# Kernel tuning notes

Hardware: AMD Instinct MI355X
Metric: run time of the kernel (lower is better)

The kernel has to match this reference:

```python
import jax, jax.numpy as jnp
import numpy as np


def _silu(x):
    return x * jax.nn.sigmoid(x)


def setup_inputs() -> dict:
    key = jax.random.key(0)
    ks = jax.random.split(key, 8)
    B, S, H, E, I, IS = 2, 1024, 2048, 64, 512, 1024
    s = 0.02  # weight init scale to keep activations in a sane range
    return {
        "hidden_states": jax.random.normal(ks[0], (B, S, H), jnp.float32),
        "gate_weight": jax.random.normal(ks[1], (E, H), jnp.float32) * s,   # router [E,H]
        "w_gate": jax.random.normal(ks[2], (E, H, I), jnp.float32) * s,
        "w_up": jax.random.normal(ks[3], (E, H, I), jnp.float32) * s,
        "w_down": jax.random.normal(ks[4], (E, I, H), jnp.float32) * s,
        "sw_gate": jax.random.normal(ks[5], (H, IS), jnp.float32) * s,
        "sw_up": jax.random.normal(ks[6], (H, IS), jnp.float32) * s,
        "sw_down": jax.random.normal(ks[7], (IS, H), jnp.float32) * s,
        "top_k": 6,
    }


def reference(hidden_states, gate_weight, w_gate, w_up, w_down,
              sw_gate, sw_up, sw_down, top_k):
    orig_shape = hidden_states.shape
    H = orig_shape[-1]
    x = hidden_states.reshape(-1, H)          # [T,H]
    T = x.shape[0]
    E = gate_weight.shape[0]

    # fp32 router (need_fp32_gate)
    logits = x.astype(jnp.float32) @ gate_weight.astype(jnp.float32).T   # [T,E]
    # sigmoid_routing_function: sigmoid -> normalize -> topk -> renormalize
    p = jax.nn.sigmoid(logits)
    p = p / jnp.sum(p, axis=-1, keepdims=True)
    topk_w, topk_idx = jax.lax.top_k(p, top_k)                           # [T,k]
    topk_w = topk_w / jnp.sum(topk_w, axis=-1, keepdims=True)            # renormalize

    # dense combine weights [T,E]: zero for unselected experts
    cw = jnp.zeros((T, E), x.dtype).at[jnp.arange(T)[:, None], topk_idx].set(
        topk_w.astype(x.dtype))

    # grouped SwiGLU expert FFN, combine weighted outputs; scan over experts
    # keeps peak memory at one [T,I] intermediate per step.
    def step(acc, ew):
        wg, wu, wd, c = ew                                               # c: [T]
        y = (_silu(x @ wg) * (x @ wu)) @ wd                              # [T,H]
        return acc + c[:, None] * y, None

    routed, _ = jax.lax.scan(step, jnp.zeros_like(x),
                             (w_gate, w_up, w_down, cw.T))

    # shared experts FFN over all tokens (returned separately, not reduced)
    shared_out = (_silu(x @ sw_gate) * (x @ sw_up)) @ sw_down            # [T,H]

    return shared_out, routed.reshape(orig_shape)
```

## Files before the change

kernel.cpp:

```cpp
#include <hip/hip_runtime.h>
#include <hip/hip_bf16.h>
#include <stdint.h>


#define H_DIM 2048
#define E_NUM 64
#define I_DIM 512
#define IS_DIM 1024
#define CAP 512
#define TOPK_MAX 8
#define BK 128
#define LDP 136

typedef float f32x4 __attribute__((ext_vector_type(4)));
typedef __bf16 bf16x8 __attribute__((ext_vector_type(8)));

__device__ __forceinline__ uint16_t f2bf(float f) {
  union { float f; uint32_t u; } v;
  v.f = f;
  uint32_t r = (v.u + 0x7FFFu + ((v.u >> 16) & 1u)) >> 16;
  return (uint16_t)r;
}
__device__ __forceinline__ uint32_t pack2(float a, float b) {
  return (uint32_t)f2bf(a) | ((uint32_t)f2bf(b) << 16);
}
__device__ __forceinline__ float bf2f(uint16_t b) {
  union { uint32_t u; float f; } v;
  v.u = (uint32_t)b << 16;
  return v.f;
}

__global__ __launch_bounds__(256) void router_kernel(
    const float* __restrict__ x, const float* __restrict__ gw,
    const int* __restrict__ topk_ptr, int* __restrict__ cnt,
    int* __restrict__ bucket, float* __restrict__ bw,
    uint16_t* __restrict__ xb) {
  const int t = blockIdx.x;
  const int tid = threadIdx.x;
  __shared__ float xs[H_DIM];
  __shared__ float logits[E_NUM];
#pragma unroll
  for (int i = 0; i < 2; ++i) {
    int idx = tid + i * 256;
    *(float4*)(&xs[idx * 4]) = *(const float4*)(x + (size_t)t * H_DIM + idx * 4);
  }
  __syncthreads();
  {
    const float* p = &xs[tid * 8];
    uint4 o;
    o.x = pack2(p[0], p[1]);
    o.y = pack2(p[2], p[3]);
    o.z = pack2(p[4], p[5]);
    o.w = pack2(p[6], p[7]);
    ((uint4*)(xb + (size_t)t * H_DIM))[tid] = o;
  }
  const int lane = tid & 63, wid = tid >> 6;
  float xr[32];
#pragma unroll
  for (int it = 0; it < 32; ++it) xr[it] = xs[lane + 64 * it];
  for (int eo = 0; eo < 16; ++eo) {
    int e = wid + eo * 4;
    const float* g = gw + (size_t)e * H_DIM;
    float acc = 0.f;
#pragma unroll
    for (int it = 0; it < 32; ++it) acc += xr[it] * g[lane + 64 * it];
#pragma unroll
    for (int off = 32; off; off >>= 1) acc += __shfl_xor(acc, off);
    if (lane == 0) logits[e] = acc;
  }
  __syncthreads();
  if (wid == 0) {
    int k = topk_ptr[0];
    if (k > TOPK_MAX) k = TOPK_MAX;
    float v = 1.f / (1.f + expf(-logits[lane]));
    float s = 0.f, myw = 0.f;
    int mye = 0;
    for (int j = 0; j < k; ++j) {
      float m = v;
      int mi = lane;
#pragma unroll
      for (int off = 32; off; off >>= 1) {
        float ov = __shfl_xor(m, off);
        int oi = __shfl_xor(mi, off);
        if (ov > m || (ov == m && oi < mi)) { m = ov; mi = oi; }
      }
      if (lane == j) { myw = m; mye = mi; }
      if (lane == mi) v = -1e30f;
      s += m;
    }
    if (lane < k) {
      float w = myw / s;
      int pos = atomicAdd(&cnt[mye], 1);
      if (pos < CAP) {
        bucket[mye * CAP + pos] = t * 8 + lane;
        bw[mye * CAP + pos] = w;
      }
    }
  }
}

template <int BM, int BN, bool GATHER>
__global__ __launch_bounds__(256) void ffn_in(
    const uint16_t* __restrict__ xb, const float* __restrict__ Wg,
    const float* __restrict__ Wu, uint16_t* __restrict__ act,
    const int* __restrict__ cnt, const int* __restrict__ bucket,
    const int K, const int ldb) {
  constexpr int MF = BM / 64;
  constexpr int NF = BN / 16;
  constexpr int CG = BN / 4;
  constexpr int PG = 256 / CG;
  constexpr int PAIRS = (BK / 2) / PG;

  int e = 0, nt, mt0, mtE, n_e;
  const float *Bg, *Bu;
  uint16_t* actE;
  if constexpr (GATHER) {
    e = blockIdx.x;
    nt = blockIdx.y;
    n_e = min(cnt[e], CAP);
    mt0 = 0;
    mtE = (n_e + BM - 1) / BM;
    const size_t wo = (size_t)e * K * ldb;
    Bg = Wg + wo;
    Bu = Wu + wo;
    actE = act + (size_t)e * CAP * ldb;
  } else {
    nt = blockIdx.x;
    mt0 = blockIdx.y;
    mtE = mt0 + 1;
    n_e = gridDim.y * BM;
    Bg = Wg;
    Bu = Wu;
    actE = act;
  }
  if (mt0 * BM >= n_e) return;

  __shared__ uint16_t Bgs[BN][LDP];
  __shared__ uint16_t Bus[BN][LDP];

  const int tid = threadIdx.x;
  const int bcol = (tid % CG) * 4, brow = tid / CG;
  const float* bgp = Bg + (size_t)(2 * brow) * ldb + nt * BN + bcol;
  const float* bup = Bu + (size_t)(2 * brow) * ldb + nt * BN + bcol;

  const int lane = tid & 63, wid = tid >> 6;
  const int fr = lane & 15, kg = lane >> 4;

  for (int mt = mt0; mt < mtE; ++mt) {
    const uint16_t* ab[MF];
#pragma unroll
    for (int mf = 0; mf < MF; ++mf) {
      const int slot = mt * BM + wid * (BM / 4) + mf * 16 + fr;
      if constexpr (GATHER) {
        const int idx = slot < n_e ? slot : 0;
        const int bv = bucket[e * CAP + idx];
        ab[mf] = xb + (size_t)(bv >> 3) * K + kg * 8;
      } else {
        ab[mf] = xb + (size_t)slot * K + kg * 8;
      }
    }

    f32x4 accg[MF][NF] = {};
    f32x4 accu[MF][NF] = {};

    float4 g0[PAIRS], g1[PAIRS], u0[PAIRS], u1[PAIRS];
#pragma unroll
    for (int pp = 0; pp < PAIRS; ++pp) {
      const float* g = bgp + (size_t)(2 * pp * PG) * ldb;
      g0[pp] = *(const float4*)g;
      g1[pp] = *(const float4*)(g + ldb);
      const float* u = bup + (size_t)(2 * pp * PG) * ldb;
      u0[pp] = *(const float4*)u;
      u1[pp] = *(const float4*)(u + ldb);
    }

    for (int k0 = 0; k0 < K; k0 += BK) {
      __syncthreads();
#pragma unroll
      for (int pp = 0; pp < PAIRS; ++pp) {
        const int rr2 = 2 * (brow + pp * PG);
        *(uint32_t*)(&Bgs[bcol + 0][rr2]) = pack2(g0[pp].x, g1[pp].x);
        *(uint32_t*)(&Bgs[bcol + 1][rr2]) = pack2(g0[pp].y, g1[pp].y);
        *(uint32_t*)(&Bgs[bcol + 2][rr2]) = pack2(g0[pp].z, g1[pp].z);
        *(uint32_t*)(&Bgs[bcol + 3][rr2]) = pack2(g0[pp].w, g1[pp].w);
        *(uint32_t*)(&Bus[bcol + 0][rr2]) = pack2(u0[pp].x, u1[pp].x);
        *(uint32_t*)(&Bus[bcol + 1][rr2]) = pack2(u0[pp].y, u1[pp].y);
        *(uint32_t*)(&Bus[bcol + 2][rr2]) = pack2(u0[pp].z, u1[pp].z);
        *(uint32_t*)(&Bus[bcol + 3][rr2]) = pack2(u0[pp].w, u1[pp].w);
      }
      __syncthreads();
      if (k0 + BK < K) {
#pragma unroll
        for (int pp = 0; pp < PAIRS; ++pp) {
          const float* g = bgp + (size_t)(k0 + BK + 2 * pp * PG) * ldb;
          g0[pp] = *(const float4*)g;
          g1[pp] = *(const float4*)(g + ldb);
          const float* u = bup + (size_t)(k0 + BK + 2 * pp * PG) * ldb;
          u0[pp] = *(const float4*)u;
          u1[pp] = *(const float4*)(u + ldb);
        }
      }
#pragma unroll
      for (int kk = 0; kk < BK / 32; ++kk) {
        bf16x8 af[MF];
#pragma unroll
        for (int mf = 0; mf < MF; ++mf)
          af[mf] = __builtin_bit_cast(
              bf16x8, *(const uint4*)(ab[mf] + k0 + kk * 32));
#pragma unroll
        for (int nf = 0; nf < NF; ++nf) {
          const bf16x8 bg = __builtin_bit_cast(
              bf16x8, *(const uint4*)(&Bgs[nf * 16 + fr][kg * 8 + kk * 32]));
          const bf16x8 bu = __builtin_bit_cast(
              bf16x8, *(const uint4*)(&Bus[nf * 16 + fr][kg * 8 + kk * 32]));
#pragma unroll
          for (int mf = 0; mf < MF; ++mf) {
            accg[mf][nf] = __builtin_amdgcn_mfma_f32_16x16x32_bf16(
                af[mf], bg, accg[mf][nf], 0, 0, 0);
            accu[mf][nf] = __builtin_amdgcn_mfma_f32_16x16x32_bf16(
                af[mf], bu, accu[mf][nf], 0, 0, 0);
          }
        }
      }
    }

#pragma unroll
    for (int mf = 0; mf < MF; ++mf)
#pragma unroll
      for (int rr = 0; rr < 4; ++rr) {
        const int slot = mt * BM + wid * (BM / 4) + mf * 16 + kg * 4 + rr;
        if (slot < n_e) {
          const size_t ro = (size_t)slot * ldb + nt * BN + fr;
#pragma unroll
          for (int nf = 0; nf < NF; ++nf) {
            const float g = accg[mf][nf][rr], u = accu[mf][nf][rr];
            actE[ro + nf * 16] = f2bf(g / (1.f + expf(-g)) * u);
          }
        }
      }
  }
}

template <int BM, int BN, bool GATHER>
__global__ __launch_bounds__(256) void ffn_down(
    const uint16_t* __restrict__ act, const float* __restrict__ Wd,
    void* __restrict__ outp, const int* __restrict__ cnt,
    const int* __restrict__ bucket, const float* __restrict__ bw, const int K) {
  constexpr int MF = BM / 64;
  constexpr int NF = BN / 16;
  constexpr int CG = BN / 4;
  constexpr int PG = 256 / CG;
  constexpr int PAIRS = (BK / 2) / PG;

  int e = 0, nt, mt0, mtE, n_e;
  const float* Bd;
  const uint16_t* actE;
  if constexpr (GATHER) {
    e = blockIdx.x;
    nt = blockIdx.y;
    n_e = min(cnt[e], CAP);
    mt0 = 0;
    mtE = (n_e + BM - 1) / BM;
    actE = act + (size_t)e * CAP * K;
    Bd = Wd + (size_t)e * K * H_DIM;
  } else {
    nt = blockIdx.x;
    mt0 = blockIdx.y;
    mtE = mt0 + 1;
    n_e = gridDim.y * BM;
    actE = act;
    Bd = Wd;
  }
  if (mt0 * BM >= n_e) return;

  __shared__ uint16_t Bs[BN][LDP];

  const int tid = threadIdx.x;
  const int bcol = (tid % CG) * 4, brow = tid / CG;
  const float* bdp = Bd + (size_t)(2 * brow) * H_DIM + nt * BN + bcol;

  const int lane = tid & 63, wid = tid >> 6;
  const int fr = lane & 15, kg = lane >> 4;

  for (int mt = mt0; mt < mtE; ++mt) {
    const uint16_t* ab[MF];
#pragma unroll
    for (int mf = 0; mf < MF; ++mf) {
      const int slot = mt * BM + wid * (BM / 4) + mf * 16 + fr;
      const int idx = slot < n_e ? slot : 0;
      ab[mf] = actE + (size_t)idx * K + kg * 8;
    }

    f32x4 acc[MF][NF] = {};

    float4 d0[PAIRS], d1[PAIRS];
#pragma unroll
    for (int pp = 0; pp < PAIRS; ++pp) {
      const float* d = bdp + (size_t)(2 * pp * PG) * H_DIM;
      d0[pp] = *(const float4*)d;
      d1[pp] = *(const float4*)(d + H_DIM);
    }

    for (int k0 = 0; k0 < K; k0 += BK) {
      __syncthreads();
#pragma unroll
      for (int pp = 0; pp < PAIRS; ++pp) {
        const int rr2 = 2 * (brow + pp * PG);
        *(uint32_t*)(&Bs[bcol + 0][rr2]) = pack2(d0[pp].x, d1[pp].x);
        *(uint32_t*)(&Bs[bcol + 1][rr2]) = pack2(d0[pp].y, d1[pp].y);
        *(uint32_t*)(&Bs[bcol + 2][rr2]) = pack2(d0[pp].z, d1[pp].z);
        *(uint32_t*)(&Bs[bcol + 3][rr2]) = pack2(d0[pp].w, d1[pp].w);
      }
      __syncthreads();
      if (k0 + BK < K) {
#pragma unroll
        for (int pp = 0; pp < PAIRS; ++pp) {
          const float* d = bdp + (size_t)(k0 + BK + 2 * pp * PG) * H_DIM;
          d0[pp] = *(const float4*)d;
          d1[pp] = *(const float4*)(d + H_DIM);
        }
      }
#pragma unroll
      for (int kk = 0; kk < BK / 32; ++kk) {
        bf16x8 af[MF];
#pragma unroll
        for (int mf = 0; mf < MF; ++mf)
          af[mf] = __builtin_bit_cast(
              bf16x8, *(const uint4*)(ab[mf] + k0 + kk * 32));
#pragma unroll
        for (int nf = 0; nf < NF; ++nf) {
          const bf16x8 bf_ = __builtin_bit_cast(
              bf16x8, *(const uint4*)(&Bs[nf * 16 + fr][kg * 8 + kk * 32]));
#pragma unroll
          for (int mf = 0; mf < MF; ++mf)
            acc[mf][nf] = __builtin_amdgcn_mfma_f32_16x16x32_bf16(
                af[mf], bf_, acc[mf][nf], 0, 0, 0);
        }
      }
    }

    const int col0 = nt * BN + fr;
#pragma unroll
    for (int mf = 0; mf < MF; ++mf)
#pragma unroll
      for (int rr = 0; rr < 4; ++rr) {
        const int slot = mt * BM + wid * (BM / 4) + mf * 16 + kg * 4 + rr;
        if constexpr (GATHER) {
          if (slot < n_e) {
            const int bv = bucket[e * CAP + slot];
            const float w = bw[e * CAP + slot];
            uint16_t* yb = (uint16_t*)outp + (size_t)bv * H_DIM + col0;
#pragma unroll
            for (int nf = 0; nf < NF; ++nf)
              yb[nf * 16] = f2bf(w * acc[mf][nf][rr]);
          }
        } else {
          float* op = (float*)outp + (size_t)slot * H_DIM + col0;
#pragma unroll
          for (int nf = 0; nf < NF; ++nf) op[nf * 16] = acc[mf][nf][rr];
        }
      }
  }
}

__global__ __launch_bounds__(256) void gather_kernel(
    const uint16_t* __restrict__ ybuf, const int* __restrict__ topk_ptr,
    float* __restrict__ routed) {
  const int t = blockIdx.x;
  const int tid = threadIdx.x;
  int k = topk_ptr[0];
  if (k > TOPK_MAX) k = TOPK_MAX;
  float acc[8] = {};
  const uint16_t* base = ybuf + (size_t)t * 8 * H_DIM + tid * 8;
  for (int j = 0; j < k; ++j) {
    uint4 v = *(const uint4*)(base + (size_t)j * H_DIM);
    const uint16_t* h = (const uint16_t*)&v;
#pragma unroll
    for (int i = 0; i < 8; ++i) acc[i] += bf2f(h[i]);
  }
  float4 o0 = make_float4(acc[0], acc[1], acc[2], acc[3]);
  float4 o1 = make_float4(acc[4], acc[5], acc[6], acc[7]);
  float* op = routed + (size_t)t * H_DIM + tid * 8;
  *(float4*)op = o0;
  *(float4*)(op + 4) = o1;
}

extern "C" void kernel_launch(void* const* d_in, const int* in_sizes, int n_in,
                              void* d_out, int out_size, void* d_ws, size_t ws_size,
                              hipStream_t stream) {
  const float* x = (const float*)d_in[0];
  const float* gw = (const float*)d_in[1];
  const float* w_gate = (const float*)d_in[2];
  const float* w_up = (const float*)d_in[3];
  const float* w_down = (const float*)d_in[4];
  const float* sw_gate = (const float*)d_in[5];
  const float* sw_up = (const float*)d_in[6];
  const float* sw_down = (const float*)d_in[7];
  const int* topk = (const int*)d_in[8];
  const int T = in_sizes[0] / H_DIM;

  float* shared_out = (float*)d_out;
  float* routed = shared_out + (size_t)T * H_DIM;

  char* ws = (char*)d_ws;
  size_t off = 0;
  auto take = [&](size_t b) {
    char* p = ws + off;
    off += (b + 255) & ~(size_t)255;
    return p;
  };
  uint16_t* xb = (uint16_t*)take((size_t)T * H_DIM * 2);
  int* cnt = (int*)take(E_NUM * 4);
  int* bucket = (int*)take((size_t)E_NUM * CAP * 4);
  float* bw = (float*)take((size_t)E_NUM * CAP * 4);
  uint16_t* act = (uint16_t*)take((size_t)E_NUM * CAP * I_DIM * 2);
  uint16_t* s_act = (uint16_t*)take((size_t)T * IS_DIM * 2);
  uint16_t* ybuf = (uint16_t*)take((size_t)T * 8 * H_DIM * 2);

  hipMemsetAsync(cnt, 0, E_NUM * 4, stream);

  router_kernel<<<T, 256, 0, stream>>>(x, gw, topk, cnt, bucket, bw, xb);

  ffn_in<256, 32, true><<<dim3(E_NUM, I_DIM / 32), 256, 0, stream>>>(
      xb, w_gate, w_up, act, cnt, bucket, H_DIM, I_DIM);
  ffn_down<256, 64, true><<<dim3(E_NUM, H_DIM / 64), 256, 0, stream>>>(
      act, w_down, (void*)ybuf, cnt, bucket, bw, I_DIM);
  gather_kernel<<<T, 256, 0, stream>>>(ybuf, topk, routed);
  ffn_in<64, 64, false><<<dim3(IS_DIM / 64, T / 64), 256, 0, stream>>>(
      xb, sw_gate, sw_up, s_act, nullptr, nullptr, H_DIM, IS_DIM);
  ffn_down<64, 128, false><<<dim3(H_DIM / 128, T / 64), 256, 0, stream>>>(
      s_act, sw_down, (void*)shared_out, nullptr, nullptr, nullptr, IS_DIM);
}
```

Baseline: 506.8 us.

## Load weight fragments directly from global memory, dropping LDS staging in FFN kernels

Removes the shared-memory staging of fp32 weights (with its pack-to-bf16 writes and two barriers per K tile). Each lane now reads its B fragment straight from global memory as 8 strided scalar fp32 loads and converts them in registers. Warps are rearranged into a 2x2 grid over M and N, and the shared-expert tile shapes and launch order change. This removes sync and LDS overhead but gives up cross-warp reuse of weight loads. The strided scalar global loads are poorly coalesced and may raise memory traffic.

```diff
diff --git a/kernel.cpp b/kernel.cpp
--- a/kernel.cpp
+++ b/kernel.cpp
@@ -9,8 +9,6 @@
 #define IS_DIM 1024
 #define CAP 512
 #define TOPK_MAX 8
-#define BK 128
-#define LDP 136
 
 typedef float f32x4 __attribute__((ext_vector_type(4)));
 typedef __bf16 bf16x8 __attribute__((ext_vector_type(8)));
@@ -105,11 +103,8 @@
     const float* __restrict__ Wu, uint16_t* __restrict__ act,
     const int* __restrict__ cnt, const int* __restrict__ bucket,
     const int K, const int ldb) {
-  constexpr int MF = BM / 64;
-  constexpr int NF = BN / 16;
-  constexpr int CG = BN / 4;
-  constexpr int PG = 256 / CG;
-  constexpr int PAIRS = (BK / 2) / PG;
+  constexpr int MF = BM / 32;
+  constexpr int NF = BN / 32;
 
   int e = 0, nt, mt0, mtE, n_e;
   const float *Bg, *Bu;
@@ -135,22 +130,19 @@
   }
   if (mt0 * BM >= n_e) return;
 
-  __shared__ uint16_t Bgs[BN][LDP];
-  __shared__ uint16_t Bus[BN][LDP];
-
   const int tid = threadIdx.x;
-  const int bcol = (tid % CG) * 4, brow = tid / CG;
-  const float* bgp = Bg + (size_t)(2 * brow) * ldb + nt * BN + bcol;
-  const float* bup = Bu + (size_t)(2 * brow) * ldb + nt * BN + bcol;
-
   const int lane = tid & 63, wid = tid >> 6;
+  const int wm = wid >> 1, wn = wid & 1;
   const int fr = lane & 15, kg = lane >> 4;
+
+  const float* bgp = Bg + (size_t)(kg * 8) * ldb + nt * BN + wn * (BN / 2) + fr;
+  const float* bup = Bu + (size_t)(kg * 8) * ldb + nt * BN + wn * (BN / 2) + fr;
 
   for (int mt = mt0; mt < mtE; ++mt) {
     const uint16_t* ab[MF];
 #pragma unroll
     for (int mf = 0; mf < MF; ++mf) {
-      const int slot = mt * BM + wid * (BM / 4) + mf * 16 + fr;
+      const int slot = mt * BM + wm * (BM / 2) + mf * 16 + fr;
       if constexpr (GATHER) {
         const int idx = slot < n_e ? slot : 0;
         const int bv = bucket[e * CAP + idx];
@@ -163,74 +155,45 @@
     f32x4 accg[MF][NF] = {};
     f32x4 accu[MF][NF] = {};
 
-    float4 g0[PAIRS], g1[PAIRS], u0[PAIRS], u1[PAIRS];
-#pragma unroll
-    for (int pp = 0; pp < PAIRS; ++pp) {
-      const float* g = bgp + (size_t)(2 * pp * PG) * ldb;
-      g0[pp] = *(const float4*)g;
-      g1[pp] = *(const float4*)(g + ldb);
-      const float* u = bup + (size_t)(2 * pp * PG) * ldb;
-      u0[pp] = *(const float4*)u;
-      u1[pp] = *(const float4*)(u + ldb);
-    }
-
-    for (int k0 = 0; k0 < K; k0 += BK) {
-      __syncthreads();
-#pragma unroll
-      for (int pp = 0; pp < PAIRS; ++pp) {
-        const int rr2 = 2 * (brow + pp * PG);
-        *(uint32_t*)(&Bgs[bcol + 0][rr2]) = pack2(g0[pp].x, g1[pp].x);
-        *(uint32_t*)(&Bgs[bcol + 1][rr2]) = pack2(g0[pp].y, g1[pp].y);
-        *(uint32_t*)(&Bgs[bcol + 2][rr2]) = pack2(g0[pp].z, g1[pp].z);
-        *(uint32_t*)(&Bgs[bcol + 3][rr2]) = pack2(g0[pp].w, g1[pp].w);
-        *(uint32_t*)(&Bus[bcol + 0][rr2]) = pack2(u0[pp].x, u1[pp].x);
-        *(uint32_t*)(&Bus[bcol + 1][rr2]) = pack2(u0[pp].y, u1[pp].y);
-        *(uint32_t*)(&Bus[bcol + 2][rr2]) = pack2(u0[pp].z, u1[pp].z);
-        *(uint32_t*)(&Bus[bcol + 3][rr2]) = pack2(u0[pp].w, u1[pp].w);
-      }
-      __syncthreads();
-      if (k0 + BK < K) {
-#pragma unroll
-        for (int pp = 0; pp < PAIRS; ++pp) {
-          const float* g = bgp + (size_t)(k0 + BK + 2 * pp * PG) * ldb;
-          g0[pp] = *(const float4*)g;
-          g1[pp] = *(const float4*)(g + ldb);
-          const float* u = bup + (size_t)(k0 + BK + 2 * pp * PG) * ldb;
-          u0[pp] = *(const float4*)u;
-          u1[pp] = *(const float4*)(u + ldb);
+#pragma unroll 2
+    for (int k0 = 0; k0 < K; k0 += 32) {
+      bf16x8 af[MF];
+#pragma unroll
+      for (int mf = 0; mf < MF; ++mf)
+        af[mf] = __builtin_bit_cast(bf16x8, *(const uint4*)(ab[mf] + k0));
+      bf16x8 bgf[NF], buf2[NF];
+#pragma unroll
+      for (int nf = 0; nf < NF; ++nf) {
+        const float* p = bgp + (size_t)k0 * ldb + nf * 16;
+        const float* q = bup + (size_t)k0 * ldb + nf * 16;
+        bf16x8 vg, vu;
+#pragma unroll
+        for (int j = 0; j < 8; ++j) {
+          vg[j] = (__bf16)p[(size_t)j * ldb];
+          vu[j] = (__bf16)q[(size_t)j * ldb];
         }
-      }
-#pragma unroll
-      for (int kk = 0; kk < BK / 32; ++kk) {
-        bf16x8 af[MF];
-#pragma unroll
-        for (int mf = 0; mf < MF; ++mf)
-          af[mf] = __builtin_bit_cast(
-              bf16x8, *(const uint4*)(ab[mf] + k0 + kk * 32));
+        bgf[nf] = vg;
+        buf2[nf] = vu;
+      }
+#pragma unroll
+      for (int mf = 0; mf < MF; ++mf)
 #pragma unroll
         for (int nf = 0; nf < NF; ++nf) {
-          const bf16x8 bg = __builtin_bit_cast(
-              bf16x8, *(const uint4*)(&Bgs[nf * 16 + fr][kg * 8 + kk * 32]));
-          const bf16x8 bu = __builtin_bit_cast(
-              bf16x8, *(const uint4*)(&Bus[nf * 16 + fr][kg * 8 + kk * 32]));
-#pragma unroll
-          for (int mf = 0; mf < MF; ++mf) {
-            accg[mf][nf] = __builtin_amdgcn_mfma_f32_16x16x32_bf16(
-                af[mf], bg, accg[mf][nf], 0, 0, 0);
-            accu[mf][nf] = __builtin_amdgcn_mfma_f32_16x16x32_bf16(
-                af[mf], bu, accu[mf][nf], 0, 0, 0);
-          }
+          accg[mf][nf] = __builtin_amdgcn_mfma_f32_16x16x32_bf16(
+              af[mf], bgf[nf], accg[mf][nf], 0, 0, 0);
+          accu[mf][nf] = __builtin_amdgcn_mfma_f32_16x16x32_bf16(
+              af[mf], buf2[nf], accu[mf][nf], 0, 0, 0);
         }
-      }
-    }
-
+    }
+
+    const int col0 = nt * BN + wn * (BN / 2) + fr;
 #pragma unroll
     for (int mf = 0; mf < MF; ++mf)
 #pragma unroll
       for (int rr = 0; rr < 4; ++rr) {
-        const int slot = mt * BM + wid * (BM / 4) + mf * 16 + kg * 4 + rr;
+        const int slot = mt * BM + wm * (BM / 2) + mf * 16 + kg * 4 + rr;
         if (slot < n_e) {
-          const size_t ro = (size_t)slot * ldb + nt * BN + fr;
+          const size_t ro = (size_t)slot * ldb + col0;
 #pragma unroll
           for (int nf = 0; nf < NF; ++nf) {
             const float g = accg[mf][nf][rr], u = accu[mf][nf][rr];
@@ -246,11 +209,8 @@
     const uint16_t* __restrict__ act, const float* __restrict__ Wd,
     void* __restrict__ outp, const int* __restrict__ cnt,
     const int* __restrict__ bucket, const float* __restrict__ bw, const int K) {
-  constexpr int MF = BM / 64;
-  constexpr int NF = BN / 16;
-  constexpr int CG = BN / 4;
-  constexpr int PG = 256 / CG;
-  constexpr int PAIRS = (BK / 2) / PG;
+  constexpr int MF = BM / 32;
+  constexpr int NF = BN / 32;
 
   int e = 0, nt, mt0, mtE, n_e;
   const float* Bd;
@@ -273,78 +233,53 @@
   }
   if (mt0 * BM >= n_e) return;
 
-  __shared__ uint16_t Bs[BN][LDP];
-
   const int tid = threadIdx.x;
-  const int bcol = (tid % CG) * 4, brow = tid / CG;
-  const float* bdp = Bd + (size_t)(2 * brow) * H_DIM + nt * BN + bcol;
-
   const int lane = tid & 63, wid = tid >> 6;
+  const int wm = wid >> 1, wn = wid & 1;
   const int fr = lane & 15, kg = lane >> 4;
+
+  const float* bdp = Bd + (size_t)(kg * 8) * H_DIM + nt * BN + wn * (BN / 2) + fr;
 
   for (int mt = mt0; mt < mtE; ++mt) {
     const uint16_t* ab[MF];
 #pragma unroll
     for (int mf = 0; mf < MF; ++mf) {
-      const int slot = mt * BM + wid * (BM / 4) + mf * 16 + fr;
+      const int slot = mt * BM + wm * (BM / 2) + mf * 16 + fr;
       const int idx = slot < n_e ? slot : 0;
       ab[mf] = actE + (size_t)idx * K + kg * 8;
     }
 
     f32x4 acc[MF][NF] = {};
 
-    float4 d0[PAIRS], d1[PAIRS];
-#pragma unroll
-    for (int pp = 0; pp < PAIRS; ++pp) {
-      const float* d = bdp + (size_t)(2 * pp * PG) * H_DIM;
-      d0[pp] = *(const float4*)d;
-      d1[pp] = *(const float4*)(d + H_DIM);
-    }
-
-    for (int k0 = 0; k0 < K; k0 += BK) {
-      __syncthreads();
-#pragma unroll
-      for (int pp = 0; pp < PAIRS; ++pp) {
-        const int rr2 = 2 * (brow + pp * PG);
-        *(uint32_t*)(&Bs[bcol + 0][rr2]) = pack2(d0[pp].x, d1[pp].x);
-        *(uint32_t*)(&Bs[bcol + 1][rr2]) = pack2(d0[pp].y, d1[pp].y);
-        *(uint32_t*)(&Bs[bcol + 2][rr2]) = pack2(d0[pp].z, d1[pp].z);
-        *(uint32_t*)(&Bs[bcol + 3][rr2]) = pack2(d0[pp].w, d1[pp].w);
-      }
-      __syncthreads();
-      if (k0 + BK < K) {
-#pragma unroll
-        for (int pp = 0; pp < PAIRS; ++pp) {
-          const float* d = bdp + (size_t)(k0 + BK + 2 * pp * PG) * H_DIM;
-          d0[pp] = *(const float4*)d;
-          d1[pp] = *(const float4*)(d + H_DIM);
-        }
-      }
-#pragma unroll
-      for (int kk = 0; kk < BK / 32; ++kk) {
-        bf16x8 af[MF];
-#pragma unroll
-        for (int mf = 0; mf < MF; ++mf)
-          af[mf] = __builtin_bit_cast(
-              bf16x8, *(const uint4*)(ab[mf] + k0 + kk * 32));
-#pragma unroll
-        for (int nf = 0; nf < NF; ++nf) {
-          const bf16x8 bf_ = __builtin_bit_cast(
-              bf16x8, *(const uint4*)(&Bs[nf * 16 + fr][kg * 8 + kk * 32]));
-#pragma unroll
-          for (int mf = 0; mf < MF; ++mf)
-            acc[mf][nf] = __builtin_amdgcn_mfma_f32_16x16x32_bf16(
-                af[mf], bf_, acc[mf][nf], 0, 0, 0);
-        }
-      }
-    }
-
-    const int col0 = nt * BN + fr;
+#pragma unroll 2
+    for (int k0 = 0; k0 < K; k0 += 32) {
+      bf16x8 af[MF];
+#pragma unroll
+      for (int mf = 0; mf < MF; ++mf)
+        af[mf] = __builtin_bit_cast(bf16x8, *(const uint4*)(ab[mf] + k0));
+      bf16x8 bdf[NF];
+#pragma unroll
+      for (int nf = 0; nf < NF; ++nf) {
+        const float* p = bdp + (size_t)k0 * H_DIM + nf * 16;
+        bf16x8 vd;
+#pragma unroll
+        for (int j = 0; j < 8; ++j) vd[j] = (__bf16)p[(size_t)j * H_DIM];
+        bdf[nf] = vd;
+      }
+#pragma unroll
+      for (int mf = 0; mf < MF; ++mf)
+#pragma unroll
+        for (int nf = 0; nf < NF; ++nf)
+          acc[mf][nf] = __builtin_amdgcn_mfma_f32_16x16x32_bf16(
+              af[mf], bdf[nf], acc[mf][nf], 0, 0, 0);
+    }
+
+    const int col0 = nt * BN + wn * (BN / 2) + fr;
 #pragma unroll
     for (int mf = 0; mf < MF; ++mf)
 #pragma unroll
       for (int rr = 0; rr < 4; ++rr) {
-        const int slot = mt * BM + wid * (BM / 4) + mf * 16 + kg * 4 + rr;
+        const int slot = mt * BM + wm * (BM / 2) + mf * 16 + kg * 4 + rr;
         if constexpr (GATHER) {
           if (slot < n_e) {
             const int bv = bucket[e * CAP + slot];
@@ -423,11 +358,11 @@
 
   ffn_in<256, 32, true><<<dim3(E_NUM, I_DIM / 32), 256, 0, stream>>>(
       xb, w_gate, w_up, act, cnt, bucket, H_DIM, I_DIM);
+  ffn_in<128, 32, false><<<dim3(IS_DIM / 32, T / 128), 256, 0, stream>>>(
+      xb, sw_gate, sw_up, s_act, nullptr, nullptr, H_DIM, IS_DIM);
   ffn_down<256, 64, true><<<dim3(E_NUM, H_DIM / 64), 256, 0, stream>>>(
       act, w_down, (void*)ybuf, cnt, bucket, bw, I_DIM);
+  ffn_down<128, 32, false><<<dim3(H_DIM / 32, T / 128), 256, 0, stream>>>(
+      s_act, sw_down, (void*)shared_out, nullptr, nullptr, nullptr, IS_DIM);
   gather_kernel<<<T, 256, 0, stream>>>(ybuf, topk, routed);
-  ffn_in<64, 64, false><<<dim3(IS_DIM / 64, T / 64), 256, 0, stream>>>(
-      xb, sw_gate, sw_up, s_act, nullptr, nullptr, H_DIM, IS_DIM);
-  ffn_down<64, 128, false><<<dim3(H_DIM / 128, T / 64), 256, 0, stream>>>(
-      s_act, sw_down, (void*)shared_out, nullptr, nullptr, nullptr, IS_DIM);
-}
+}
```

Measured after the change: 760.6 us. 1.5x slower.

## Double-buffer weight tiles in LDS with single barrier per K-step

Applied to the files above, without the earlier changes.

Converts the FFN GEMM kernels to a double-buffered LDS pipeline with BK halved to 64: the next tile is converted and written into the alternate buffer while the current one feeds MFMAs, and global loads are issued two stages ahead. Each K-step now needs one custom barrier (waitcnt on lgkm plus s_barrier) instead of two __syncthreads. The shared-expert launches also change tile shapes to 128x32 and 128x64. The early-return guard on empty tiles is removed, and the smaller K step means more loop iterations, with some extra register pressure from holding the prefetched values.

```diff
diff --git a/kernel.cpp b/kernel.cpp
--- a/kernel.cpp
+++ b/kernel.cpp
@@ -9,8 +9,8 @@
 #define IS_DIM 1024
 #define CAP 512
 #define TOPK_MAX 8
-#define BK 128
-#define LDP 136
+#define BK 64
+#define LDP 68
 
 typedef float f32x4 __attribute__((ext_vector_type(4)));
 typedef __bf16 bf16x8 __attribute__((ext_vector_type(8)));
@@ -29,6 +29,13 @@
   v.u = (uint32_t)b << 16;
   return v.f;
 }
+
+#define BAR()                                              \
+  do {                                                     \
+    asm volatile("s_waitcnt lgkmcnt(0)" ::: "memory");     \
+    __builtin_amdgcn_s_barrier();                          \
+    asm volatile("" ::: "memory");                         \
+  } while (0)
 
 __global__ __launch_bounds__(256) void router_kernel(
     const float* __restrict__ x, const float* __restrict__ gw,
@@ -109,7 +116,7 @@
   constexpr int NF = BN / 16;
   constexpr int CG = BN / 4;
   constexpr int PG = 256 / CG;
-  constexpr int PAIRS = (BK / 2) / PG;
+  constexpr int PAIRS = 32 / PG;
 
   int e = 0, nt, mt0, mtE, n_e;
   const float *Bg, *Bu;
@@ -133,19 +140,21 @@
     Bu = Wu;
     actE = act;
   }
-  if (mt0 * BM >= n_e) return;
-
-  __shared__ uint16_t Bgs[BN][LDP];
-  __shared__ uint16_t Bus[BN][LDP];
+
+  __shared__ uint16_t Bgs[2][BN][LDP];
+  __shared__ uint16_t Bus[2][BN][LDP];
 
   const int tid = threadIdx.x;
-  const int bcol = (tid % CG) * 4, brow = tid / CG;
-  const float* bgp = Bg + (size_t)(2 * brow) * ldb + nt * BN + bcol;
-  const float* bup = Bu + (size_t)(2 * brow) * ldb + nt * BN + bcol;
+  const int cg4 = (tid % CG) * 4, kp = tid / CG;
+  const float* bgp = Bg + (size_t)(2 * kp) * ldb + nt * BN + cg4;
+  const float* bup = Bu + (size_t)(2 * kp) * ldb + nt * BN + cg4;
 
   const int lane = tid & 63, wid = tid >> 6;
   const int fr = lane & 15, kg = lane >> 4;
 
+  float4 g0[PAIRS], g1[PAIRS], u0[PAIRS], u1[PAIRS];
+
+  const int NS = K / BK;
   for (int mt = mt0; mt < mtE; ++mt) {
     const uint16_t* ab[MF];
 #pragma unroll
@@ -163,7 +172,6 @@
     f32x4 accg[MF][NF] = {};
     f32x4 accu[MF][NF] = {};
 
-    float4 g0[PAIRS], g1[PAIRS], u0[PAIRS], u1[PAIRS];
 #pragma unroll
     for (int pp = 0; pp < PAIRS; ++pp) {
       const float* g = bgp + (size_t)(2 * pp * PG) * ldb;
@@ -173,64 +181,96 @@
       u0[pp] = *(const float4*)u;
       u1[pp] = *(const float4*)(u + ldb);
     }
-
-    for (int k0 = 0; k0 < K; k0 += BK) {
-      __syncthreads();
+#pragma unroll
+    for (int pp = 0; pp < PAIRS; ++pp) {
+      const int k2 = 2 * (kp + pp * PG);
+      *(uint32_t*)(&Bgs[0][cg4 + 0][k2]) = pack2(g0[pp].x, g1[pp].x);
+      *(uint32_t*)(&Bgs[0][cg4 + 1][k2]) = pack2(g0[pp].y, g1[pp].y);
+      *(uint32_t*)(&Bgs[0][cg4 + 2][k2]) = pack2(g0[pp].z, g1[pp].z);
+      *(uint32_t*)(&Bgs[0][cg4 + 3][k2]) = pack2(g0[pp].w, g1[pp].w);
+      *(uint32_t*)(&Bus[0][cg4 + 0][k2]) = pack2(u0[pp].x, u1[pp].x);
+      *(uint32_t*)(&Bus[0][cg4 + 1][k2]) = pack2(u0[pp].y, u1[pp].y);
+      *(uint32_t*)(&Bus[0][cg4 + 2][k2]) = pack2(u0[pp].z, u1[pp].z);
+      *(uint32_t*)(&Bus[0][cg4 + 3][k2]) = pack2(u0[pp].w, u1[pp].w);
+    }
+    if (NS > 1) {
 #pragma unroll
       for (int pp = 0; pp < PAIRS; ++pp) {
-        const int rr2 = 2 * (brow + pp * PG);
-        *(uint32_t*)(&Bgs[bcol + 0][rr2]) = pack2(g0[pp].x, g1[pp].x);
-        *(uint32_t*)(&Bgs[bcol + 1][rr2]) = pack2(g0[pp].y, g1[pp].y);
-        *(uint32_t*)(&Bgs[bcol + 2][rr2]) = pack2(g0[pp].z, g1[pp].z);
-        *(uint32_t*)(&Bgs[bcol + 3][rr2]) = pack2(g0[pp].w, g1[pp].w);
-        *(uint32_t*)(&Bus[bcol + 0][rr2]) = pack2(u0[pp].x, u1[pp].x);
-        *(uint32_t*)(&Bus[bcol + 1][rr2]) = pack2(u0[pp].y, u1[pp].y);
-        *(uint32_t*)(&Bus[bcol + 2][rr2]) = pack2(u0[pp].z, u1[pp].z);
-        *(uint32_t*)(&Bus[bcol + 3][rr2]) = pack2(u0[pp].w, u1[pp].w);
-      }
-      __syncthreads();
-      if (k0 + BK < K) {
+        const float* g = bgp + (size_t)(BK + 2 * pp * PG) * ldb;
+        g0[pp] = *(const float4*)g;
+        g1[pp] = *(const float4*)(g + ldb);
+        const float* u = bup + (size_t)(BK + 2 * pp * PG) * ldb;
+        u0[pp] = *(const float4*)u;
+        u1[pp] = *(const float4*)(u + ldb);
+      }
+    }
+    BAR();
+
+    int b = 0;
+    for (int s = 0; s < NS; ++s) {
+      const int k0 = s * BK;
+      uint4 a[MF][2];
+#pragma unroll
+      for (int mf = 0; mf < MF; ++mf)
+#pragma unroll
+        for (int sl = 0; sl < 2; ++sl)
+          a[mf][sl] = *(const uint4*)(ab[mf] + k0 + sl * 32);
+      if (s + 1 < NS) {
 #pragma unroll
         for (int pp = 0; pp < PAIRS; ++pp) {
-          const float* g = bgp + (size_t)(k0 + BK + 2 * pp * PG) * ldb;
+          const int k2 = 2 * (kp + pp * PG);
+          *(uint32_t*)(&Bgs[b ^ 1][cg4 + 0][k2]) = pack2(g0[pp].x, g1[pp].x);
+          *(uint32_t*)(&Bgs[b ^ 1][cg4 + 1][k2]) = pack2(g0[pp].y, g1[pp].y);
+          *(uint32_t*)(&Bgs[b ^ 1][cg4 + 2][k2]) = pack2(g0[pp].z, g1[pp].z);
+          *(uint32_t*)(&Bgs[b ^ 1][cg4 + 3][k2]) = pack2(g0[pp].w, g1[pp].w);
+          *(uint32_t*)(&Bus[b ^ 1][cg4 + 0][k2]) = pack2(u0[pp].x, u1[pp].x);
+          *(uint32_t*)(&Bus[b ^ 1][cg4 + 1][k2]) = pack2(u0[pp].y, u1[pp].y);
+          *(uint32_t*)(&Bus[b ^ 1][cg4 + 2][k2]) = pack2(u0[pp].z, u1[pp].z);
+          *(uint32_t*)(&Bus[b ^ 1][cg4 + 3][k2]) = pack2(u0[pp].w, u1[pp].w);
+        }
+      }
+      if (s + 2 < NS) {
+        const int kq = k0 + 2 * BK;
+#pragma unroll
+        for (int pp = 0; pp < PAIRS; ++pp) {
+          const float* g = bgp + (size_t)(kq + 2 * pp * PG) * ldb;
           g0[pp] = *(const float4*)g;
           g1[pp] = *(const float4*)(g + ldb);
-          const float* u = bup + (size_t)(k0 + BK + 2 * pp * PG) * ldb;
+          const float* u = bup + (size_t)(kq + 2 * pp * PG) * ldb;
           u0[pp] = *(const float4*)u;
           u1[pp] = *(const float4*)(u + ldb);
         }
       }
 #pragma unroll
-      for (int kk = 0; kk < BK / 32; ++kk) {
-        bf16x8 af[MF];
-#pragma unroll
-        for (int mf = 0; mf < MF; ++mf)
-          af[mf] = __builtin_bit_cast(
-              bf16x8, *(const uint4*)(ab[mf] + k0 + kk * 32));
+      for (int sl = 0; sl < 2; ++sl) {
 #pragma unroll
         for (int nf = 0; nf < NF; ++nf) {
           const bf16x8 bg = __builtin_bit_cast(
-              bf16x8, *(const uint4*)(&Bgs[nf * 16 + fr][kg * 8 + kk * 32]));
+              bf16x8, *(const uint4*)(&Bgs[b][nf * 16 + fr][kg * 8 + sl * 32]));
           const bf16x8 bu = __builtin_bit_cast(
-              bf16x8, *(const uint4*)(&Bus[nf * 16 + fr][kg * 8 + kk * 32]));
+              bf16x8, *(const uint4*)(&Bus[b][nf * 16 + fr][kg * 8 + sl * 32]));
 #pragma unroll
           for (int mf = 0; mf < MF; ++mf) {
+            const bf16x8 af = __builtin_bit_cast(bf16x8, a[mf][sl]);
             accg[mf][nf] = __builtin_amdgcn_mfma_f32_16x16x32_bf16(
-                af[mf], bg, accg[mf][nf], 0, 0, 0);
+                af, bg, accg[mf][nf], 0, 0, 0);
             accu[mf][nf] = __builtin_amdgcn_mfma_f32_16x16x32_bf16(
-                af[mf], bu, accu[mf][nf], 0, 0, 0);
+                af, bu, accu[mf][nf], 0, 0, 0);
           }
         }
       }
-    }
-
+      BAR();
+      b ^= 1;
+    }
+
+    const int col0 = nt * BN + fr;
 #pragma unroll
     for (int mf = 0; mf < MF; ++mf)
 #pragma unroll
       for (int rr = 0; rr < 4; ++rr) {
         const int slot = mt * BM + wid * (BM / 4) + mf * 16 + kg * 4 + rr;
         if (slot < n_e) {
-          const size_t ro = (size_t)slot * ldb + nt * BN + fr;
+          const size_t ro = (size_t)slot * ldb + col0;
 #pragma unroll
           for (int nf = 0; nf < NF; ++nf) {
             const float g = accg[mf][nf][rr], u = accu[mf][nf][rr];
@@ -250,7 +290,7 @@
   constexpr int NF = BN / 16;
   constexpr int CG = BN / 4;
   constexpr int PG = 256 / CG;
-  constexpr int PAIRS = (BK / 2) / PG;
+  constexpr int PAIRS = 32 / PG;
 
   int e = 0, nt, mt0, mtE, n_e;
   const float* Bd;
@@ -271,16 +311,18 @@
     actE = act;
     Bd = Wd;
   }
-  if (mt0 * BM >= n_e) return;
-
-  __shared__ uint16_t Bs[BN][LDP];
+
+  __shared__ uint16_t Bs[2][BN][LDP];
 
   const int tid = threadIdx.x;
-  const int bcol = (tid % CG) * 4, brow = tid / CG;
-  const float* bdp = Bd + (size_t)(2 * brow) * H_DIM + nt * BN + bcol;
+  const int cg4 = (tid % CG) * 4, kp = tid / CG;
+  const float* bdp = Bd + (size_t)(2 * kp) * H_DIM + nt * BN + cg4;
 
   const int lane = tid & 63, wid = tid >> 6;
   const int fr = lane & 15, kg = lane >> 4;
+
+  float4 d0[PAIRS], d1[PAIRS];
+  const int NS = K / BK;
 
   for (int mt = mt0; mt < mtE; ++mt) {
     const uint16_t* ab[MF];
@@ -293,50 +335,74 @@
 
     f32x4 acc[MF][NF] = {};
 
-    float4 d0[PAIRS], d1[PAIRS];
 #pragma unroll
     for (int pp = 0; pp < PAIRS; ++pp) {
       const float* d = bdp + (size_t)(2 * pp * PG) * H_DIM;
       d0[pp] = *(const float4*)d;
       d1[pp] = *(const float4*)(d + H_DIM);
     }
-
-    for (int k0 = 0; k0 < K; k0 += BK) {
-      __syncthreads();
+#pragma unroll
+    for (int pp = 0; pp < PAIRS; ++pp) {
+      const int k2 = 2 * (kp + pp * PG);
+      *(uint32_t*)(&Bs[0][cg4 + 0][k2]) = pack2(d0[pp].x, d1[pp].x);
+      *(uint32_t*)(&Bs[0][cg4 + 1][k2]) = pack2(d0[pp].y, d1[pp].y);
+      *(uint32_t*)(&Bs[0][cg4 + 2][k2]) = pack2(d0[pp].z, d1[pp].z);
+      *(uint32_t*)(&Bs[0][cg4 + 3][k2]) = pack2(d0[pp].w, d1[pp].w);
+    }
+    if (NS > 1) {
 #pragma unroll
       for (int pp = 0; pp < PAIRS; ++pp) {
-        const int rr2 = 2 * (brow + pp * PG);
-        *(uint32_t*)(&Bs[bcol + 0][rr2]) = pack2(d0[pp].x, d1[pp].x);
-        *(uint32_t*)(&Bs[bcol + 1][rr2]) = pack2(d0[pp].y, d1[pp].y);
-        *(uint32_t*)(&Bs[bcol + 2][rr2]) = pack2(d0[pp].z, d1[pp].z);
-        *(uint32_t*)(&Bs[bcol + 3][rr2]) = pack2(d0[pp].w, d1[pp].w);
-      }
-      __syncthreads();
-      if (k0 + BK < K) {
+        const float* d = bdp + (size_t)(BK + 2 * pp * PG) * H_DIM;
+        d0[pp] = *(const float4*)d;
+        d1[pp] = *(const float4*)(d + H_DIM);
+      }
+    }
+    BAR();
+
+    int b = 0;
+    for (int s = 0; s < NS; ++s) {
+      const int k0 = s * BK;
+      uint4 a[MF][2];
+#pragma unroll
+      for (int mf = 0; mf < MF; ++mf)
+#pragma unroll
+        for (int sl = 0; sl < 2; ++sl)
+          a[mf][sl] = *(const uint4*)(ab[mf] + k0 + sl * 32);
+      if (s + 1 < NS) {
 #pragma unroll
         for (int pp = 0; pp < PAIRS; ++pp) {
-          const float* d = bdp + (size_t)(k0 + BK + 2 * pp * PG) * H_DIM;
+          const int k2 = 2 * (kp + pp * PG);
+          *(uint32_t*)(&Bs[b ^ 1][cg4 + 0][k2]) = pack2(d0[pp].x, d1[pp].x);
+          *(uint32_t*)(&Bs[b ^ 1][cg4 + 1][k2]) = pack2(d0[pp].y, d1[pp].y);
+          *(uint32_t*)(&Bs[b ^ 1][cg4 + 2][k2]) = pack2(d0[pp].z, d1[pp].z);
+          *(uint32_t*)(&Bs[b ^ 1][cg4 + 3][k2]) = pack2(d0[pp].w, d1[pp].w);
+        }
+      }
+      if (s + 2 < NS) {
+        const int kq = k0 + 2 * BK;
+#pragma unroll
+        for (int pp = 0; pp < PAIRS; ++pp) {
+          const float* d = bdp + (size_t)(kq + 2 * pp * PG) * H_DIM;
           d0[pp] = *(const float4*)d;
           d1[pp] = *(const float4*)(d + H_DIM);
         }
       }
 #pragma unroll
-      for (int kk = 0; kk < BK / 32; ++kk) {
-        bf16x8 af[MF];
-#pragma unroll
-        for (int mf = 0; mf < MF; ++mf)
-          af[mf] = __builtin_bit_cast(
-              bf16x8, *(const uint4*)(ab[mf] + k0 + kk * 32));
+      for (int sl = 0; sl < 2; ++sl) {
 #pragma unroll
         for (int nf = 0; nf < NF; ++nf) {
           const bf16x8 bf_ = __builtin_bit_cast(
-              bf16x8, *(const uint4*)(&Bs[nf * 16 + fr][kg * 8 + kk * 32]));
-#pragma unroll
-          for (int mf = 0; mf < MF; ++mf)
+              bf16x8, *(const uint4*)(&Bs[b][nf * 16 + fr][kg * 8 + sl * 32]));
+#pragma unroll
+          for (int mf = 0; mf < MF; ++mf) {
+            const bf16x8 af = __builtin_bit_cast(bf16x8, a[mf][sl]);
             acc[mf][nf] = __builtin_amdgcn_mfma_f32_16x16x32_bf16(
-                af[mf], bf_, acc[mf][nf], 0, 0, 0);
-        }
-      }
+                af, bf_, acc[mf][nf], 0, 0, 0);
+          }
+        }
+      }
+      BAR();
+      b ^= 1;
     }
 
     const int col0 = nt * BN + fr;
@@ -426,8 +492,8 @@
   ffn_down<256, 64, true><<<dim3(E_NUM, H_DIM / 64), 256, 0, stream>>>(
       act, w_down, (void*)ybuf, cnt, bucket, bw, I_DIM);
   gather_kernel<<<T, 256, 0, stream>>>(ybuf, topk, routed);
-  ffn_in<64, 64, false><<<dim3(IS_DIM / 64, T / 64), 256, 0, stream>>>(
+  ffn_in<128, 32, false><<<dim3(IS_DIM / 32, T / 128), 256, 0, stream>>>(
       xb, sw_gate, sw_up, s_act, nullptr, nullptr, H_DIM, IS_DIM);
-  ffn_down<64, 128, false><<<dim3(H_DIM / 128, T / 64), 256, 0, stream>>>(
+  ffn_down<128, 64, false><<<dim3(H_DIM / 64, T / 128), 256, 0, stream>>>(
       s_act, sw_down, (void*)shared_out, nullptr, nullptr, nullptr, IS_DIM);
 }
```

New measurement: 431.9 us. -14.8%, faster.
